# Kernel optimization log

Measured on AMD Instinct MI355X. Metric: run time of the kernel, lower is better.

Reference implementation:

```python
import jax, jax.numpy as jnp
import numpy as np

D_MODEL = 768
N_HEADS = 12
D_FF = 3072
EPS = 1e-6


def _xavier(key, shape):
    fan_out, fan_in = shape
    a = jnp.sqrt(6.0 / (fan_in + fan_out))
    return jax.random.uniform(key, shape, jnp.float32, -a, a)


def setup_inputs() -> dict:
    key = jax.random.key(0)
    ks = jax.random.split(key, 10)
    B, S = 2, 2048
    x = jax.random.normal(ks[0], (B, S, D_MODEL), jnp.float32)
    mask = jax.random.randint(ks[1], (B, 1, 1, S), 0, 2) == 1
    wq = _xavier(ks[2], (D_MODEL, D_MODEL)); bq = jnp.zeros((D_MODEL,))
    wk = _xavier(ks[3], (D_MODEL, D_MODEL)); bk = jnp.zeros((D_MODEL,))
    wv = _xavier(ks[4], (D_MODEL, D_MODEL)); bv = jnp.zeros((D_MODEL,))
    wo = _xavier(ks[5], (D_MODEL, D_MODEL)); bo = jnp.zeros((D_MODEL,))
    w1 = _xavier(ks[6], (D_FF, D_MODEL)); b1 = jnp.zeros((D_FF,))
    w2 = _xavier(ks[7], (D_MODEL, D_FF)); b2 = jnp.zeros((D_MODEL,))
    g1 = jnp.ones((D_MODEL,)); be1 = jnp.zeros((D_MODEL,))
    g2 = jnp.ones((D_MODEL,)); be2 = jnp.zeros((D_MODEL,))
    return dict(x=x, mask=mask, wq=wq, bq=bq, wk=wk, bk=bk, wv=wv, bv=bv,
                wo=wo, bo=bo, w1=w1, b1=b1, w2=w2, b2=b2,
                g1=g1, be1=be1, g2=g2, be2=be2)


def _layer_norm(x, gamma, beta):
    # torch: mean + unbiased std (ddof=1), divide by (std + eps)
    mean = jnp.mean(x, axis=-1, keepdims=True)
    std = jnp.std(x, axis=-1, keepdims=True, ddof=1)
    return gamma * (x - mean) / (std + EPS) + beta


def _encoder(x, mask, wq, bq, wk, bk, wv, bv, wo, bo, w1, b1, w2, b2, g1, be1, g2, be2):
    B, S, D = x.shape
    H, Dk = N_HEADS, D // N_HEADS
    q = (x @ wq.T + bq).reshape(B, S, H, Dk).transpose(0, 2, 1, 3)
    k = (x @ wk.T + bk).reshape(B, S, H, Dk).transpose(0, 2, 1, 3)
    v = (x @ wv.T + bv).reshape(B, S, H, Dk).transpose(0, 2, 1, 3)
    scores = jnp.einsum('bhqd,bhkd->bhqk', q, k) / jnp.sqrt(jnp.float32(Dk))
    scores = jnp.where(mask, jnp.float32(-1e9), scores)
    probs = jax.nn.softmax(scores, axis=-1)
    attn = jnp.einsum('bhqk,bhkd->bhqd', probs, v)
    attn = attn.transpose(0, 2, 1, 3).reshape(B, S, D)
    attn = attn @ wo.T + bo
    x = _layer_norm(x + attn, g1, be1)
    ff = jax.nn.relu(x @ w1.T + b1) @ w2.T + b2
    return _layer_norm(x + ff, g2, be2)


def reference(x, mask, wq, bq, wk, bk, wv, bv, wo, bo, w1, b1, w2, b2, g1, be1, g2, be2):
    return _encoder(x, mask, wq, bq, wk, bk, wv, bv, wo, bo, w1, b1, w2, b2, g1, be1, g2, be2)
```

## Files before the change

### kernel.cpp

```cpp
#include <hip/hip_runtime.h>
#include <hip/hip_bf16.h>

typedef __hip_bfloat16 bf16;
typedef unsigned short ushort;
typedef __attribute__((ext_vector_type(8))) short short8;
typedef __attribute__((ext_vector_type(4))) float f32x4;

__device__ __forceinline__ float b2f(bf16 h) { return __bfloat162float(h); }
__device__ __forceinline__ bf16 f2b(float f) { return __float2bfloat16(f); }
__device__ __forceinline__ ushort f2bu(float f) {
    bf16 t = __float2bfloat16(f);
    ushort u;
    __builtin_memcpy(&u, &t, 2);
    return u;
}
__device__ __forceinline__ float bits2f(unsigned int u16) {
    unsigned int v = u16 << 16;
    float f;
    __builtin_memcpy(&f, &v, 4);
    return f;
}

__device__ __forceinline__ void gload16(const void* g, void* l) {
    __builtin_amdgcn_global_load_lds(
        (const __attribute__((address_space(1))) void*)g,
        (__attribute__((address_space(3))) void*)l, 16, 0, 0);
}

__global__ void detect_dtype_kernel(const unsigned short* __restrict__ x,
                                    int* __restrict__ flag) {
    __shared__ int cnt;
    if (threadIdx.x == 0) cnt = 0;
    __syncthreads();
    int local = 0;
    for (int i = threadIdx.x; i < 2048; i += 256) {
        float v = bits2f((unsigned int)x[i]);
        if (!(fabsf(v) < 1e4f)) local++;
    }
    atomicAdd(&cnt, local);
    __syncthreads();
    if (threadIdx.x == 0) flag[0] = (cnt >= 8) ? 1 : 0;
}

__device__ __forceinline__ void load8f_rt(const void* p, int isf, float* f) {
    if (isf) {
        const float* q = (const float*)p;
        float4 a = *(const float4*)q;
        float4 b = *(const float4*)(q + 4);
        f[0] = a.x; f[1] = a.y; f[2] = a.z; f[3] = a.w;
        f[4] = b.x; f[5] = b.y; f[6] = b.z; f[7] = b.w;
    } else {
        uint4 u = *(const uint4*)p;
        f[0] = bits2f(u.x & 0xffffu); f[1] = bits2f(u.x >> 16);
        f[2] = bits2f(u.y & 0xffffu); f[3] = bits2f(u.y >> 16);
        f[4] = bits2f(u.z & 0xffffu); f[5] = bits2f(u.z >> 16);
        f[6] = bits2f(u.w & 0xffffu); f[7] = bits2f(u.w >> 16);
    }
}
__device__ __forceinline__ float loadf_rt(const void* p, int isf, size_t i) {
    return isf ? ((const float*)p)[i] : bits2f(((const ushort*)p)[i]);
}

__global__ __launch_bounds__(256) void conv_all_k(
    const int* __restrict__ dflag,
    const void* __restrict__ x,
    const void* __restrict__ wq, const void* __restrict__ wk,
    const void* __restrict__ wv, const void* __restrict__ wo,
    const void* __restrict__ w1, const void* __restrict__ w2,
    const void* __restrict__ bq, const void* __restrict__ bk,
    const void* __restrict__ bv, const void* __restrict__ bo,
    const void* __restrict__ b1, const void* __restrict__ b2,
    const void* __restrict__ g1, const void* __restrict__ be1,
    const void* __restrict__ g2, const void* __restrict__ be2,
    ushort* __restrict__ xb, ushort* __restrict__ wall,
    float* __restrict__ vall)
{
    const int isf = dflag[0];
    const int esz = isf ? 4 : 2;
    const int gt = blockIdx.x * 256 + threadIdx.x;
    const int stride = gridDim.x * 256;

    for (int v = gt; v < 393216; v += stride) {
        float f[8];
        load8f_rt((const char*)x + (size_t)v * 8 * esz, isf, f);
        unsigned int wd[4];
        #pragma unroll
        for (int i = 0; i < 4; ++i)
            wd[i] = (unsigned int)f2bu(f[2 * i]) | ((unsigned int)f2bu(f[2 * i + 1]) << 16);
        *(uint4*)(xb + (size_t)v * 8) = make_uint4(wd[0], wd[1], wd[2], wd[3]);
    }
    for (int v = gt; v < 884736; v += stride) {
        const void* src; int loc;
        if (v < 73728)        { src = wq; loc = v; }
        else if (v < 147456)  { src = wk; loc = v - 73728; }
        else if (v < 221184)  { src = wv; loc = v - 147456; }
        else if (v < 294912)  { src = wo; loc = v - 221184; }
        else if (v < 589824)  { src = w1; loc = v - 294912; }
        else                  { src = w2; loc = v - 589824; }
        float f[8];
        load8f_rt((const char*)src + (size_t)loc * 8 * esz, isf, f);
        unsigned int wd[4];
        #pragma unroll
        for (int i = 0; i < 4; ++i)
            wd[i] = (unsigned int)f2bu(f[2 * i]) | ((unsigned int)f2bu(f[2 * i + 1]) << 16);
        *(uint4*)(wall + (size_t)v * 8) = make_uint4(wd[0], wd[1], wd[2], wd[3]);
    }
    for (int i = gt; i < 9984; i += stride) {
        const void* s; int l;
        if (i < 768)       { s = bq;  l = i; }
        else if (i < 1536) { s = bk;  l = i - 768; }
        else if (i < 2304) { s = bv;  l = i - 1536; }
        else if (i < 3072) { s = bo;  l = i - 2304; }
        else if (i < 6144) { s = b1;  l = i - 3072; }
        else if (i < 6912) { s = b2;  l = i - 6144; }
        else if (i < 7680) { s = g1;  l = i - 6912; }
        else if (i < 8448) { s = be1; l = i - 7680; }
        else if (i < 9216) { s = g2;  l = i - 8448; }
        else               { s = be2; l = i - 9216; }
        vall[i] = loadf_rt(s, isf, l);
    }
}

template <int BM>
__device__ __forceinline__ void gemm_bf16_body(
    const ushort* __restrict__ A, const ushort* __restrict__ Bw,
    const float* __restrict__ bias, ushort* __restrict__ Cb,
    float* __restrict__ Cf, int N, int K, int kstart, int klen,
    int bm, int bn, int relu)
{
    __shared__ __align__(16) ushort As[2][BM][64];
    __shared__ __align__(16) ushort Bs[2][128][64];
    const int tid = threadIdx.x;
    const int w = tid >> 6, lane = tid & 63;
    const int quad = lane >> 4, l15 = lane & 15;
    constexpr int FM = BM / 32;
    const int wr = (w >> 1) * (BM / 2), wc = (w & 1) * 64;

    constexpr int CA = (BM * 128) / 4096;
    constexpr int CB = 4;
    size_t aoff[CA]; int albase[CA];
    #pragma unroll
    for (int c = 0; c < CA; ++c) {
        int byte = c * 4096 + tid * 16;
        int row = byte >> 7, colb = byte & 127;
        int csrc = colb ^ ((row & 7) << 4);
        aoff[c] = (size_t)(bm + row) * K + (csrc >> 1);
        albase[c] = c * 4096 + w * 1024;
    }
    size_t boff[CB]; int blbase[CB];
    #pragma unroll
    for (int c = 0; c < CB; ++c) {
        int byte = c * 4096 + tid * 16;
        int row = byte >> 7, colb = byte & 127;
        int csrc = colb ^ ((row & 7) << 4);
        boff[c] = (size_t)(bn + row) * K + (csrc >> 1);
        blbase[c] = c * 4096 + w * 1024;
    }

    f32x4 acc[FM][4];
    #pragma unroll
    for (int i = 0; i < FM; ++i)
        #pragma unroll
        for (int j = 0; j < 4; ++j) acc[i][j] = (f32x4){0.f, 0.f, 0.f, 0.f};

    constexpr int ASZ = BM * 128;
    constexpr int BSZ = 128 * 128;

#define STAGE(buf, k0)                                                        \
    {                                                                         \
        char* ab = (char*)As + (buf) * ASZ;                                   \
        char* bb = (char*)Bs + (buf) * BSZ;                                   \
        _Pragma("unroll")                                                     \
        for (int c = 0; c < CA; ++c)                                          \
            gload16(A + aoff[c] + (k0), ab + albase[c]);                      \
        _Pragma("unroll")                                                     \
        for (int c = 0; c < CB; ++c)                                          \
            gload16(Bw + boff[c] + (k0), bb + blbase[c]);                     \
    }

    const int NT = klen >> 6;
    STAGE(0, kstart);
    int cur = 0;
    for (int t = 0; t < NT; ++t) {
        __syncthreads();
        if (t + 1 < NT) STAGE(cur ^ 1, kstart + (t + 1) * 64);

        const ushort (*Asb)[64] = As[cur];
        const ushort (*Bsb)[64] = Bs[cur];
        short8 af[FM][2], bfr[4][2];
        #pragma unroll
        for (int i = 0; i < FM; ++i) {
            int r = wr + i * 16 + l15;
            int sw = (r & 7) << 3;
            af[i][0] = *(const short8*)&Asb[r][(quad * 8) ^ sw];
            af[i][1] = *(const short8*)&Asb[r][(32 + quad * 8) ^ sw];
        }
        #pragma unroll
        for (int j = 0; j < 4; ++j) {
            int r = wc + j * 16 + l15;
            int sw = (r & 7) << 3;
            bfr[j][0] = *(const short8*)&Bsb[r][(quad * 8) ^ sw];
            bfr[j][1] = *(const short8*)&Bsb[r][(32 + quad * 8) ^ sw];
        }
        #pragma unroll
        for (int h = 0; h < 2; ++h)
            #pragma unroll
            for (int i = 0; i < FM; ++i)
                #pragma unroll
                for (int j = 0; j < 4; ++j)
                    acc[i][j] = __builtin_amdgcn_mfma_f32_16x16x32_bf16(
                        af[i][h], bfr[j][h], acc[i][j], 0, 0, 0);
        cur ^= 1;
    }
#undef STAGE

    #pragma unroll
    for (int j = 0; j < 4; ++j) {
        int col = bn + wc + j * 16 + l15;
        float bv = bias ? bias[col] : 0.f;
        #pragma unroll
        for (int i = 0; i < FM; ++i) {
            int row0 = bm + wr + i * 16 + quad * 4;
            #pragma unroll
            for (int r = 0; r < 4; ++r) {
                float vv = acc[i][j][r] + bv;
                if (relu) vv = fmaxf(vv, 0.f);
                size_t idx = (size_t)(row0 + r) * N + col;
                if (Cb) Cb[idx] = f2bu(vv);
                if (Cf) Cf[idx] = vv;
            }
        }
    }
}

__device__ __forceinline__ int xcd_swz(int bid, int nwg) {
    int cpx = nwg >> 3;
    return (bid & 7) * cpx + (bid >> 3);
}

template <int BM>
__global__ __launch_bounds__(256) void gemm_b(
    const ushort* __restrict__ A, const ushort* __restrict__ Bw,
    const float* __restrict__ bias, ushort* __restrict__ Cb,
    float* __restrict__ Cf, int N, int K, int relu)
{
    int nwg = gridDim.x * gridDim.y;
    int bid = xcd_swz(blockIdx.y * gridDim.x + blockIdx.x, nwg);
    int bx = bid % gridDim.x, by = bid / gridDim.x;
    gemm_bf16_body<BM>(A, Bw, bias, Cb, Cf, N, K, 0, K, by * BM, bx * 128, relu);
}

template <int BM>
__global__ __launch_bounds__(256) void gemm_ksplit(
    const ushort* __restrict__ A, const ushort* __restrict__ Bw,
    const float* __restrict__ bias, float* __restrict__ Cf, int N, int K)
{
    const int part = blockIdx.z;
    int nwg = gridDim.x * gridDim.y;
    int bid = xcd_swz(blockIdx.y * gridDim.x + blockIdx.x, nwg);
    int bx = bid % gridDim.x, by = bid / gridDim.x;
    const int kh = K >> 1;
    gemm_bf16_body<BM>(A, Bw, part ? nullptr : bias, nullptr,
                       Cf + (size_t)part * 3145728, N, K,
                       part * kh, kh, by * BM, bx * 128, 0);
}

__global__ __launch_bounds__(256) void gemm_qkv_b(
    const ushort* __restrict__ x, const ushort* __restrict__ wall,
    const float* __restrict__ vall,
    ushort* __restrict__ qb, ushort* __restrict__ kb, ushort* __restrict__ vb)
{
    int bid = xcd_swz(blockIdx.y * 18 + blockIdx.x, 576);
    int bx = bid % 18, by = bid / 18;
    const int mat = bx / 6;
    const int bn = (bx % 6) * 128;
    const ushort* W = wall + (size_t)mat * 589824;
    const float* Bi = vall + mat * 768;
    ushort* O = (mat == 0) ? qb : (mat == 1) ? kb : vb;
    gemm_bf16_body<128>(x, W, Bi, O, nullptr, 768, 768, 0, 768, by * 128, bn, 0);
}

template <int NP>
__global__ __launch_bounds__(512) void attn_mfma_b(
    const ushort* __restrict__ q, const ushort* __restrict__ k,
    const ushort* __restrict__ v, const int* __restrict__ mask,
    float* __restrict__ opart, float* __restrict__ mlbuf)
{
    const int S = 2048, D = 768;
    constexpr int SPK = 2048 / NP;
    constexpr int NT = SPK / 64;
    const size_t NXD = 3145728;
    const float SC2 = 0.125f * 1.44269504088896f;
    __shared__ __align__(16) ushort Ks[64][72];
    __shared__ __align__(16) ushort Vt[64][72];
    __shared__ __align__(16) ushort Ps[8][16][72];
    __shared__ float mkAll[SPK];

    const int tid = threadIdx.x;
    const int w = tid >> 6, lane = tid & 63;
    const int quad = lane >> 4, l15 = lane & 15;

    const int bx = xcd_swz(blockIdx.x, NP * 384);
    const int part = bx / 384;
    const int rest = bx - part * 384;
    const int q0 = (rest & 15) * 128;
    const int h = (rest >> 4) % 12;
    const int b = rest / 192;
    const int kbase = part * SPK;

    #pragma unroll
    for (int i = 0; i < SPK / 512; ++i) {
        int idx = tid + i * 512;
        mkAll[idx] = mask[b * S + kbase + idx] ? -30000.f : 0.f;
    }

    const size_t qrow = (size_t)(b * S + q0 + w * 16 + l15) * D + h * 64;
    const short8 aQ0 = *(const short8*)&q[qrow + quad * 8];
    const short8 aQ1 = *(const short8*)&q[qrow + 32 + quad * 8];

    short8 ones;
    #pragma unroll
    for (int j = 0; j < 8; ++j) ones[j] = (short)0x3F80;

    f32x4 o[4], lacc;
    #pragma unroll
    for (int i = 0; i < 4; ++i) o[i] = (f32x4){0.f, 0.f, 0.f, 0.f};
    lacc = (f32x4){0.f, 0.f, 0.f, 0.f};
    float m_run = -3.0e38f;

    const int sr = tid >> 3;
    const int sc0 = (tid & 7) * 8;

    const ushort* kp = k + (size_t)(b * S + kbase + sr) * D + h * 64 + sc0;
    const ushort* vp = v + (size_t)(b * S + kbase + lane) * D + h * 64 + w * 8;
    uint4 ka = *(const uint4*)kp;
    uint4 va = *(const uint4*)vp;

    for (int kt = 0; kt < NT; ++kt) {
        __syncthreads();
        *(uint4*)&Ks[sr][sc0] = ka;
        {
            alignas(16) ushort tmp[8];
            *(uint4*)tmp = va;
            #pragma unroll
            for (int i = 0; i < 8; ++i) Vt[w * 8 + i][lane] = tmp[i];
        }
        __syncthreads();

        if (kt + 1 < NT) {
            kp += 64 * D;
            vp += 64 * D;
            ka = *(const uint4*)kp;
            va = *(const uint4*)vp;
        }

        const float* mk = &mkAll[kt * 64];
        float scv[4][4];
        float vm = -3.0e38f;
        __builtin_amdgcn_s_setprio(1);
        #pragma unroll
        for (int s = 0; s < 4; ++s) {
            short8 bk0 = *(const short8*)&Ks[s * 16 + l15][quad * 8];
            short8 bk1 = *(const short8*)&Ks[s * 16 + l15][32 + quad * 8];
            f32x4 c = (f32x4){0.f, 0.f, 0.f, 0.f};
            c = __builtin_amdgcn_mfma_f32_16x16x32_bf16(aQ0, bk0, c, 0, 0, 0);
            c = __builtin_amdgcn_mfma_f32_16x16x32_bf16(aQ1, bk1, c, 0, 0, 0);
            float mb = mk[s * 16 + l15];
            #pragma unroll
            for (int r = 0; r < 4; ++r) {
                float val = __builtin_fmaf(c[r], SC2, mb);
                scv[s][r] = val;
                vm = fmaxf(vm, val);
            }
        }
        __builtin_amdgcn_s_setprio(0);
        vm = fmaxf(vm, __shfl_xor(vm, 1, 16));
        vm = fmaxf(vm, __shfl_xor(vm, 2, 16));
        vm = fmaxf(vm, __shfl_xor(vm, 4, 16));
        vm = fmaxf(vm, __shfl_xor(vm, 8, 16));

        if (__any(vm > m_run + 11.0f)) {
            float mn = fmaxf(m_run, vm);
            float alpha = exp2f(m_run - mn);
            #pragma unroll
            for (int s = 0; s < 4; ++s) o[s] *= alpha;
            lacc *= alpha;
            m_run = mn;
        }

        #pragma unroll
        for (int r = 0; r < 4; ++r)
            #pragma unroll
            for (int s = 0; s < 4; ++s)
                Ps[w][quad * 4 + r][(s * 16 + l15) ^ (quad << 4)] =
                    f2bu(exp2f(scv[s][r] - m_run));
        asm volatile("s_waitcnt lgkmcnt(0)" ::: "memory");

        {
            const int pswz = (l15 >> 2) << 4;
            short8 aP0 = *(const short8*)&Ps[w][l15][(quad * 8) ^ pswz];
            short8 aP1 = *(const short8*)&Ps[w][l15][(32 + quad * 8) ^ pswz];
            __builtin_amdgcn_s_setprio(1);
            lacc = __builtin_amdgcn_mfma_f32_16x16x32_bf16(aP0, ones, lacc, 0, 0, 0);
            lacc = __builtin_amdgcn_mfma_f32_16x16x32_bf16(aP1, ones, lacc, 0, 0, 0);
            #pragma unroll
            for (int s = 0; s < 4; ++s) {
                short8 bv0 = *(const short8*)&Vt[s * 16 + l15][quad * 8];
                short8 bv1 = *(const short8*)&Vt[s * 16 + l15][32 + quad * 8];
                o[s] = __builtin_amdgcn_mfma_f32_16x16x32_bf16(aP0, bv0, o[s], 0, 0, 0);
                o[s] = __builtin_amdgcn_mfma_f32_16x16x32_bf16(aP1, bv1, o[s], 0, 0, 0);
            }
            __builtin_amdgcn_s_setprio(0);
        }
    }

    const size_t obase = (size_t)part * NXD +
                         (size_t)(b * S + q0 + w * 16) * D + h * 64;
    #pragma unroll
    for (int r = 0; r < 4; ++r)
        #pragma unroll
        for (int s = 0; s < 4; ++s)
            opart[obase + (size_t)(quad * 4 + r) * D + s * 16 + l15] = o[s][r];
    if (l15 == 0) {
        #pragma unroll
        for (int r = 0; r < 4; ++r) {
            int row = b * S + q0 + w * 16 + quad * 4 + r;
            size_t mi = (((size_t)part * 4096 + row) * 12 + h) * 2;
            mlbuf[mi] = m_run;
            mlbuf[mi + 1] = lacc[r];
        }
    }
}

template <int NP>
__global__ __launch_bounds__(256) void attn_combine(
    const float* __restrict__ opart, const float* __restrict__ mlbuf,
    ushort* __restrict__ ctx)
{
    const size_t NXD = 3145728;
    const int row = blockIdx.x;
    const int tid = threadIdx.x;
    #pragma unroll
    for (int i = 0; i < 3; ++i) {
        int d = tid + i * 256;
        int h = d >> 6;
        float mv[NP], lv[NP];
        float m = -3.0e38f;
        #pragma unroll
        for (int p = 0; p < NP; ++p) {
            size_t mi = (((size_t)p * 4096 + row) * 12 + h) * 2;
            mv[p] = mlbuf[mi];
            lv[p] = mlbuf[mi + 1];
            m = fmaxf(m, mv[p]);
        }
        size_t idx = (size_t)row * 768 + d;
        float den = 0.f, num = 0.f;
        #pragma unroll
        for (int p = 0; p < NP; ++p) {
            float e = exp2f(mv[p] - m);
            den += lv[p] * e;
            num += opart[(size_t)p * NXD + idx] * e;
        }
        ctx[idx] = f2bu(num / den);
    }
}

__global__ __launch_bounds__(256) void ln1_kernel(
    const int* __restrict__ dflag,
    const void* __restrict__ xa, const float* __restrict__ r0,
    const float* __restrict__ r1,
    const float* __restrict__ gamma, const float* __restrict__ beta,
    ushort* __restrict__ outb, float* __restrict__ outf)
{
    const int isf = dflag[0];
    const int row = blockIdx.x;
    const int tid = threadIdx.x;
    __shared__ float red[4];
    const size_t base = (size_t)row * 768;

    float x[3];
    #pragma unroll
    for (int i = 0; i < 3; ++i) {
        int d = tid + i * 256;
        x[i] = loadf_rt(xa, isf, base + d) + r0[base + d] + r1[base + d];
    }

    float s = x[0] + x[1] + x[2];
    #pragma unroll
    for (int off = 32; off > 0; off >>= 1) s += __shfl_down(s, off, 64);
    if ((tid & 63) == 0) red[tid >> 6] = s;
    __syncthreads();
    float mean = (red[0] + red[1] + red[2] + red[3]) * (1.f / 768.f);
    __syncthreads();

    float vsum = 0.f;
    #pragma unroll
    for (int i = 0; i < 3; ++i) {
        float dd = x[i] - mean;
        vsum += dd * dd;
    }
    #pragma unroll
    for (int off = 32; off > 0; off >>= 1) vsum += __shfl_down(vsum, off, 64);
    if ((tid & 63) == 0) red[tid >> 6] = vsum;
    __syncthreads();
    float var = (red[0] + red[1] + red[2] + red[3]) * (1.f / 767.f);
    float inv = 1.f / (sqrtf(var) + 1e-6f);

    #pragma unroll
    for (int i = 0; i < 3; ++i) {
        int d = tid + i * 256;
        float y = gamma[d] * (x[i] - mean) * inv + beta[d];
        outb[base + d] = f2bu(y);
        outf[base + d] = y;
    }
}

__global__ __launch_bounds__(256) void ln2_kernel(
    const int* __restrict__ dflag,
    const float* __restrict__ a, const float* __restrict__ f0,
    const float* __restrict__ f1,
    const float* __restrict__ gamma, const float* __restrict__ beta,
    void* __restrict__ out)
{
    const int isf = dflag[0];
    const int row = blockIdx.x;
    const int tid = threadIdx.x;
    __shared__ float red[4];
    const size_t base = (size_t)row * 768;

    float x[3];
    #pragma unroll
    for (int i = 0; i < 3; ++i) {
        int d = tid + i * 256;
        x[i] = a[base + d] + f0[base + d] + f1[base + d];
    }

    float s = x[0] + x[1] + x[2];
    #pragma unroll
    for (int off = 32; off > 0; off >>= 1) s += __shfl_down(s, off, 64);
    if ((tid & 63) == 0) red[tid >> 6] = s;
    __syncthreads();
    float mean = (red[0] + red[1] + red[2] + red[3]) * (1.f / 768.f);
    __syncthreads();

    float vsum = 0.f;
    #pragma unroll
    for (int i = 0; i < 3; ++i) {
        float dd = x[i] - mean;
        vsum += dd * dd;
    }
    #pragma unroll
    for (int off = 32; off > 0; off >>= 1) vsum += __shfl_down(vsum, off, 64);
    if ((tid & 63) == 0) red[tid >> 6] = vsum;
    __syncthreads();
    float var = (red[0] + red[1] + red[2] + red[3]) * (1.f / 767.f);
    float inv = 1.f / (sqrtf(var) + 1e-6f);

    #pragma unroll
    for (int i = 0; i < 3; ++i) {
        int d = tid + i * 256;
        float y = gamma[d] * (x[i] - mean) * inv + beta[d];
        if (isf) ((float*)out)[base + d] = y;
        else     ((ushort*)out)[base + d] = f2bu(y);
    }
}

extern "C" void kernel_launch(void* const* d_in, const int* in_sizes, int n_in,
                              void* d_out, int out_size, void* d_ws, size_t ws_size,
                              hipStream_t stream) {
    const size_t nxd = 3145728;
    char* base = (char*)d_ws;
    int* dflag = (int*)base;

    char* p = base + 256;
    ushort* xb   = (ushort*)p; p += nxd * 2;
    ushort* wall = (ushort*)p; p += 7077888ull * 2;
    float*  vall = (float*)p;  p += 40960;
    ushort* qb   = (ushort*)p;
    ushort* kb   = qb + nxd;
    ushort* vb   = kb + nxd;
    ushort* ctx  = vb + nxd;
    ushort* ff1b = qb;
    p += 4 * nxd * 2;
    float* dbuf = (float*)p; p += nxd * 4;
    float* ebuf = (float*)p; p += nxd * 4;
    float* fbuf = (float*)p; p += nxd * 4;
    float* gbuf = (float*)p; p += nxd * 4;
    float* mbuf = (float*)p; p += 4 * 4096 * 12 * 2 * 4;
    size_t need4 = (size_t)((char*)(mbuf + 393216) - base);

    float* opart = dbuf;
    ushort* ln1b = xb;
    float* ln1f = gbuf;

    const int* mask = (const int*)d_in[1];
    dim3 blk(256);

    detect_dtype_kernel<<<dim3(1), blk, 0, stream>>>(
        (const unsigned short*)d_in[0], dflag);

    conv_all_k<<<dim3(1024), blk, 0, stream>>>(dflag,
        d_in[0], d_in[2], d_in[4], d_in[6], d_in[8], d_in[10], d_in[12],
        d_in[3], d_in[5], d_in[7], d_in[9], d_in[11], d_in[13],
        d_in[14], d_in[15], d_in[16], d_in[17], xb, wall, vall);

    gemm_qkv_b<<<dim3(18, 32), blk, 0, stream>>>(xb, wall, vall, qb, kb, vb);

    if (ws_size >= need4) {
        attn_mfma_b<4><<<dim3(1536), dim3(512), 0, stream>>>(
            qb, kb, vb, mask, opart, mbuf);
        attn_combine<4><<<dim3(4096), blk, 0, stream>>>(opart, mbuf, ctx);
    } else {
        attn_mfma_b<2><<<dim3(768), dim3(512), 0, stream>>>(
            qb, kb, vb, mask, opart, gbuf);
        attn_combine<2><<<dim3(4096), blk, 0, stream>>>(opart, gbuf, ctx);
    }

    gemm_ksplit<64><<<dim3(6, 64, 2), blk, 0, stream>>>(
        ctx, wall + 1769472, vall + 2304, dbuf, 768, 768);

    ln1_kernel<<<dim3(4096), blk, 0, stream>>>(dflag,
        d_in[0], dbuf, ebuf, vall + 6912, vall + 7680, ln1b, ln1f);

    gemm_b<128><<<dim3(24, 32), blk, 0, stream>>>(
        ln1b, wall + 2359296, vall + 3072, ff1b, nullptr, 3072, 768, 1);

    gemm_ksplit<64><<<dim3(6, 64, 2), blk, 0, stream>>>(
        ff1b, wall + 4718592, vall + 6144, dbuf, 768, 3072);

    ln2_kernel<<<dim3(4096), blk, 0, stream>>>(dflag,
        ln1f, dbuf, ebuf, vall + 8448, vall + 9216, d_out);
}
```

Baseline: 312.4 us.

## Double-buffer K/V tiles via async global-to-LDS loads and fix split to 2

The attention kernel now stages K and V tiles straight into double-buffered, XOR-swizzled LDS with global_load_lds, prefetching the next tile during compute instead of holding it in registers. One of the two __syncthreads per tile becomes a single s_barrier placed after the P writes. The host always launches the 2-way key split, dropping the 4-way path and its extra workspace. This cuts register pressure and barriers, but adds LDS usage and may lower occupancy or parallelism from fewer blocks.

```diff
diff --git a/kernel.cpp b/kernel.cpp
--- a/kernel.cpp
+++ b/kernel.cpp
@@ -291,7 +291,8 @@
     constexpr int NT = SPK / 64;
     const size_t NXD = 3145728;
     const float SC2 = 0.125f * 1.44269504088896f;
-    __shared__ __align__(16) ushort Ks[64][72];
+    __shared__ __align__(16) ushort Ks2[2][64][64];
+    __shared__ __align__(16) ushort Vs2[2][64][64];
     __shared__ __align__(16) ushort Vt[64][72];
     __shared__ __align__(16) ushort Ps[8][16][72];
     __shared__ float mkAll[SPK];
@@ -328,30 +329,34 @@
     lacc = (f32x4){0.f, 0.f, 0.f, 0.f};
     float m_run = -3.0e38f;
 
-    const int sr = tid >> 3;
-    const int sc0 = (tid & 7) * 8;
-
-    const ushort* kp = k + (size_t)(b * S + kbase + sr) * D + h * 64 + sc0;
-    const ushort* vp = v + (size_t)(b * S + kbase + lane) * D + h * 64 + w * 8;
-    uint4 ka = *(const uint4*)kp;
-    uint4 va = *(const uint4*)vp;
-
+    const int srow = tid >> 3;
+    const int scol = ((tid & 7) * 8) ^ ((srow & 7) << 3);
+    const ushort* ksrc = k + (size_t)(b * S + kbase + srow) * D + h * 64 + scol;
+    const ushort* vsrc = v + (size_t)(b * S + kbase + srow) * D + h * 64 + scol;
+    char* KsB = (char*)Ks2;
+    char* VsB = (char*)Vs2;
+    const int wb = w * 1024;
+
+#define STAGE_KV(bb, kt0)                                                     \
+    {                                                                         \
+        gload16(ksrc + (size_t)(kt0) * 64 * 768, KsB + (bb) * 8192 + wb);     \
+        gload16(vsrc + (size_t)(kt0) * 64 * 768, VsB + (bb) * 8192 + wb);     \
+    }
+
+    STAGE_KV(0, 0);
+    int cur = 0;
     for (int kt = 0; kt < NT; ++kt) {
         __syncthreads();
-        *(uint4*)&Ks[sr][sc0] = ka;
+
+        if (kt + 1 < NT) STAGE_KV(cur ^ 1, kt + 1);
+
         {
+            const int c = (w * 8) ^ ((lane & 7) << 3);
+            short8 tv = *(const short8*)&Vs2[cur][lane][c];
             alignas(16) ushort tmp[8];
-            *(uint4*)tmp = va;
+            *(short8*)tmp = tv;
             #pragma unroll
             for (int i = 0; i < 8; ++i) Vt[w * 8 + i][lane] = tmp[i];
-        }
-        __syncthreads();
-
-        if (kt + 1 < NT) {
-            kp += 64 * D;
-            vp += 64 * D;
-            ka = *(const uint4*)kp;
-            va = *(const uint4*)vp;
         }
 
         const float* mk = &mkAll[kt * 64];
@@ -360,8 +365,10 @@
         __builtin_amdgcn_s_setprio(1);
         #pragma unroll
         for (int s = 0; s < 4; ++s) {
-            short8 bk0 = *(const short8*)&Ks[s * 16 + l15][quad * 8];
-            short8 bk1 = *(const short8*)&Ks[s * 16 + l15][32 + quad * 8];
+            int krow = s * 16 + l15;
+            int ksw = (krow & 7) << 3;
+            short8 bk0 = *(const short8*)&Ks2[cur][krow][(quad * 8) ^ ksw];
+            short8 bk1 = *(const short8*)&Ks2[cur][krow][(32 + quad * 8) ^ ksw];
             f32x4 c = (f32x4){0.f, 0.f, 0.f, 0.f};
             c = __builtin_amdgcn_mfma_f32_16x16x32_bf16(aQ0, bk0, c, 0, 0, 0);
             c = __builtin_amdgcn_mfma_f32_16x16x32_bf16(aQ1, bk1, c, 0, 0, 0);
@@ -394,7 +401,11 @@
             for (int s = 0; s < 4; ++s)
                 Ps[w][quad * 4 + r][(s * 16 + l15) ^ (quad << 4)] =
                     f2bu(exp2f(scv[s][r] - m_run));
+
         asm volatile("s_waitcnt lgkmcnt(0)" ::: "memory");
+        __builtin_amdgcn_sched_barrier(0);
+        __builtin_amdgcn_s_barrier();
+        __builtin_amdgcn_sched_barrier(0);
 
         {
             const int pswz = (l15 >> 2) << 4;
@@ -412,7 +423,10 @@
             }
             __builtin_amdgcn_s_setprio(0);
         }
-    }
+
+        cur ^= 1;
+    }
+#undef STAGE_KV
 
     const size_t obase = (size_t)part * NXD +
                          (size_t)(b * S + q0 + w * 16) * D + h * 64;
@@ -584,12 +598,10 @@
     p += 4 * nxd * 2;
     float* dbuf = (float*)p; p += nxd * 4;
     float* ebuf = (float*)p; p += nxd * 4;
-    float* fbuf = (float*)p; p += nxd * 4;
     float* gbuf = (float*)p; p += nxd * 4;
-    float* mbuf = (float*)p; p += 4 * 4096 * 12 * 2 * 4;
-    size_t need4 = (size_t)((char*)(mbuf + 393216) - base);
 
     float* opart = dbuf;
+    float* mlbuf = gbuf;
     ushort* ln1b = xb;
     float* ln1f = gbuf;
 
@@ -606,15 +618,9 @@
 
     gemm_qkv_b<<<dim3(18, 32), blk, 0, stream>>>(xb, wall, vall, qb, kb, vb);
 
-    if (ws_size >= need4) {
-        attn_mfma_b<4><<<dim3(1536), dim3(512), 0, stream>>>(
-            qb, kb, vb, mask, opart, mbuf);
-        attn_combine<4><<<dim3(4096), blk, 0, stream>>>(opart, mbuf, ctx);
-    } else {
-        attn_mfma_b<2><<<dim3(768), dim3(512), 0, stream>>>(
-            qb, kb, vb, mask, opart, gbuf);
-        attn_combine<2><<<dim3(4096), blk, 0, stream>>>(opart, gbuf, ctx);
-    }
+    attn_mfma_b<2><<<dim3(768), dim3(512), 0, stream>>>(
+        qb, kb, vb, mask, opart, mlbuf);
+    attn_combine<2><<<dim3(4096), blk, 0, stream>>>(opart, mlbuf, ctx);
 
     gemm_ksplit<64><<<dim3(6, 64, 2), blk, 0, stream>>>(
         ctx, wall + 1769472, vall + 2304, dbuf, 768, 768);
```

New measurement: 325.6 us. +4.2%, slower.
